# Optimization experiments

Measured on AMD Instinct MI355X. Metric: run time of the kernel, lower is better.

The kernel has to match this reference:

```python
import jax, jax.numpy as jnp
import numpy as np

EMB_DIM = 256
Q_DIM = 512
V_DIM = 512

def setup_inputs() -> dict:
    key = jax.random.key(0)
    ks = jax.random.split(key, 7)
    B, S = 8, 2048
    x = jax.random.normal(ks[0], (B, S, EMB_DIM), dtype=jnp.float32)
    s = 1.0 / np.sqrt(EMB_DIM)
    Wq = jax.random.normal(ks[1], (EMB_DIM, Q_DIM), dtype=jnp.float32) * s
    bq = jax.random.normal(ks[2], (Q_DIM,), dtype=jnp.float32) * 0.01
    Wk = jax.random.normal(ks[3], (EMB_DIM, Q_DIM), dtype=jnp.float32) * s
    bk = jax.random.normal(ks[4], (Q_DIM,), dtype=jnp.float32) * 0.01
    Wv = jax.random.normal(ks[5], (EMB_DIM, V_DIM), dtype=jnp.float32) * s
    bv = jax.random.normal(ks[6], (V_DIM,), dtype=jnp.float32) * 0.01
    return {"x": x, "Wq": Wq, "bq": bq, "Wk": Wk, "bk": bk, "Wv": Wv, "bv": bv}

def reference(x, Wq, bq, Wk, bk, Wv, bv):
    # q/k/v projections (torch Linear == x @ W + b with W stored [in, out] here)
    q = jax.nn.sigmoid(jnp.einsum('bse,eq->bsq', x, Wq) + bq)   # [B,S,Q]
    k = jnp.einsum('bse,eq->bsq', x, Wk) + bk                   # [B,S,Q]
    v = jnp.einsum('bse,ev->bsv', x, Wv) + bv                   # [B,S,V]
    scale = 1.0 / jnp.sqrt(jnp.float32(EMB_DIM))
    qk = jnp.einsum('bsq,btq->bst', q, k) * scale               # [B,S,S]
    qk = jax.nn.elu(qk)
    attn = jax.nn.softmax(qk, axis=-1)
    return jnp.einsum('bst,btv->bsv', attn, v)                  # [B,S,V]
```

## Files before the change

### kernel.cpp

```cpp
#include <hip/hip_runtime.h>
#include <hip/hip_bf16.h>
#include <math.h>

typedef unsigned short u16;
using short8 = __attribute__((ext_vector_type(8))) short;
using f32x4  = __attribute__((ext_vector_type(4))) float;

#define BK 32


__device__ __forceinline__ u16 f2bf(float f) {
  union { float f; unsigned u; } v; v.f = f;
  unsigned r = v.u + 0x7FFFu + ((v.u >> 16) & 1u);
  return (u16)(r >> 16);
}

__device__ __forceinline__ float fexp(float x) { return __expf(x); }

__device__ __forceinline__ void gld16(const void* g, void* l) {
  __builtin_amdgcn_global_load_lds(
      (const __attribute__((address_space(1))) void*)g,
      (__attribute__((address_space(3))) void*)l,
      16, 0, 0);
}


__device__ __forceinline__ void gemm_core4(const u16* __restrict__ Ag,
                                           const u16* __restrict__ Bg,
                                           int K, int lda, int ldb,
                                           u16* As, u16* Bs,
                                           f32x4 acc[4][4], int w, int l) {
  const int wm = (w & 1) << 6, wn = (w >> 1) << 6;
  const int ln = l & 15, lq = l >> 4;
  const int sr0 = w * 16 + (l >> 2);
  const int sr1 = 64 + sr0;
  const int skp = (l & 3) * 8;
  const int skg = ((l & 3) ^ ((l >> 3) & 3)) * 8;
  const int kro = (lq ^ ((ln >> 1) & 3)) * 8;

#pragma unroll
  for (int mt = 0; mt < 4; mt++)
#pragma unroll
    for (int nt = 0; nt < 4; nt++) acc[mt][nt] = (f32x4)0.0f;

  for (int k0 = 0; k0 < K; k0 += BK) {
    __syncthreads();
    gld16(Ag + (size_t)sr0 * lda + k0 + skg, As + sr0 * BK + skp);
    gld16(Ag + (size_t)sr1 * lda + k0 + skg, As + sr1 * BK + skp);
    gld16(Bg + (size_t)sr0 * ldb + k0 + skg, Bs + sr0 * BK + skp);
    gld16(Bg + (size_t)sr1 * ldb + k0 + skg, Bs + sr1 * BK + skp);
    __syncthreads();
    short8 af[4], bf[4];
#pragma unroll
    for (int mt = 0; mt < 4; mt++)
      af[mt] = *(const short8*)(As + (wm + mt * 16 + ln) * BK + kro);
#pragma unroll
    for (int nt = 0; nt < 4; nt++)
      bf[nt] = *(const short8*)(Bs + (wn + nt * 16 + ln) * BK + kro);
#pragma unroll
    for (int mt = 0; mt < 4; mt++)
#pragma unroll
      for (int nt = 0; nt < 4; nt++)
        acc[mt][nt] = __builtin_amdgcn_mfma_f32_16x16x32_bf16(
            af[mt], bf[nt], acc[mt][nt], 0, 0, 0);
  }
}


__global__ __launch_bounds__(256) void k_conv(
    const float* __restrict__ x, u16* __restrict__ xb,
    const float* __restrict__ Wq, const float* __restrict__ Wk,
    const float* __restrict__ Wv, const float* __restrict__ bq,
    const float* __restrict__ bk, const float* __restrict__ bv,
    u16* __restrict__ Wt, float* __restrict__ bcat,
    float* __restrict__ lsum) {
  const int bid = blockIdx.x;
  if (bid < 4096) {
    int i = bid * 256 + threadIdx.x;
    float4 v = ((const float4*)x)[i];
    ushort4 o;
    o.x = f2bf(v.x); o.y = f2bf(v.y); o.z = f2bf(v.z); o.w = f2bf(v.w);
    ((ushort4*)xb)[i] = o;
  } else if (bid < 5632) {
    int i = (bid - 4096) * 256 + threadIdx.x;
    int nn = i >> 8, e = i & 255;
    int sel = nn >> 9, c = nn & 511;
    const float* W = (sel == 0) ? Wq : (sel == 1) ? Wk : Wv;
    Wt[i] = f2bf(W[e * 512 + c]);
    if (e == 0) {
      const float* bb = (sel == 0) ? bq : (sel == 1) ? bk : bv;
      bcat[nn] = bb[c];
    }
  } else {
    int i = (bid - 5632) * 256 + threadIdx.x;
    lsum[i] = 0.0f;
  }
}


__global__ __launch_bounds__(256) void k_proj(
    const u16* __restrict__ xb, const u16* __restrict__ Wt,
    const float* __restrict__ bcat, u16* __restrict__ qb,
    u16* __restrict__ kb, u16* __restrict__ vtb) {
  __shared__ __align__(16) u16 As8[8 * 4096];
  __shared__ __align__(16) u16 Bs[4096];
  const int bm = blockIdx.y * 128;
  const int bnq = blockIdx.x;
  const int tid = threadIdx.x, w = tid >> 6, l = tid & 63;
  const int wm = (w & 1) << 6, wn = (w >> 1) << 6;
  const int ln = l & 15, lq = l >> 4;
  const int sr0 = w * 16 + (l >> 2);
  const int sr1 = 64 + sr0;
  const int skp = (l & 3) * 8;
  const int skg = ((l & 3) ^ ((l >> 3) & 3)) * 8;
  const int kro = (lq ^ ((ln >> 1) & 3)) * 8;

#pragma unroll
  for (int kw = 0; kw < 8; kw++) {
    gld16(xb + (size_t)(bm + sr0) * 256 + kw * 32 + skg,
          As8 + kw * 4096 + sr0 * BK + skp);
    gld16(xb + (size_t)(bm + sr1) * 256 + kw * 32 + skg,
          As8 + kw * 4096 + sr1 * BK + skp);
  }

  const int b = bm >> 11, t0 = bm & 2047;
  const int cb = bnq * 128;

  for (int p = 0; p < 3; p++) {
    const u16* Bg = Wt + (size_t)(p * 512 + cb) * 256;
    f32x4 acc[4][4];
#pragma unroll
    for (int mt = 0; mt < 4; mt++)
#pragma unroll
      for (int nt = 0; nt < 4; nt++) acc[mt][nt] = (f32x4)0.0f;

#pragma unroll
    for (int it = 0; it < 8; it++) {
      __syncthreads();
      gld16(Bg + (size_t)sr0 * 256 + it * 32 + skg, Bs + sr0 * BK + skp);
      gld16(Bg + (size_t)sr1 * 256 + it * 32 + skg, Bs + sr1 * BK + skp);
      __syncthreads();
      const u16* Aw = As8 + it * 4096;
      short8 af[4], bf[4];
#pragma unroll
      for (int mt = 0; mt < 4; mt++)
        af[mt] = *(const short8*)(Aw + (wm + mt * 16 + ln) * BK + kro);
#pragma unroll
      for (int nt = 0; nt < 4; nt++)
        bf[nt] = *(const short8*)(Bs + (wn + nt * 16 + ln) * BK + kro);
#pragma unroll
      for (int mt = 0; mt < 4; mt++)
#pragma unroll
        for (int nt = 0; nt < 4; nt++)
          acc[mt][nt] = __builtin_amdgcn_mfma_f32_16x16x32_bf16(
              af[mt], bf[nt], acc[mt][nt], 0, 0, 0);
    }

    if (p < 2) {
      u16* dst = p ? kb : qb;
#pragma unroll
      for (int mt = 0; mt < 4; mt++)
#pragma unroll
        for (int r = 0; r < 4; r++) {
          int row = bm + wm + mt * 16 + lq * 4 + r;
#pragma unroll
          for (int nt = 0; nt < 4; nt++) {
            int col = wn + nt * 16 + ln;
            float v = acc[mt][nt][r] + bcat[p * 512 + cb + col];
            float ov = (p == 0) ? __builtin_amdgcn_rcpf(1.0f + fexp(-v)) : v;
            dst[(size_t)row * 512 + cb + col] = f2bf(ov);
          }
        }
    } else {
      u16* tr = As8;
#pragma unroll
      for (int h = 0; h < 2; h++) {
        __syncthreads();
        if ((w & 1) == h) {
#pragma unroll
          for (int mt = 0; mt < 4; mt++)
#pragma unroll
            for (int nt = 0; nt < 4; nt++) {
              int c = wn + nt * 16 + ln;
              float bias = bcat[1024 + cb + c];
#pragma unroll
              for (int r = 0; r < 4; r++) {
                int lr = mt * 16 + lq * 4 + r;
                tr[c * 68 + lr] = f2bf(acc[mt][nt][r] + bias);
              }
            }
        }
        __syncthreads();
        int c2 = tid >> 1, half = tid & 1;
        size_t dbase = ((size_t)b * 512 + cb + c2) * 2048 + t0 + h * 64 + half * 32;
#pragma unroll
        for (int j = 0; j < 4; j++) {
          ushort4 a0 = *(const ushort4*)&tr[c2 * 68 + half * 32 + j * 8];
          ushort4 a1 = *(const ushort4*)&tr[c2 * 68 + half * 32 + j * 8 + 4];
          *(ushort4*)&vtb[dbase + j * 8] = a0;
          *(ushort4*)&vtb[dbase + j * 8 + 4] = a1;
        }
      }
    }
  }
}


__global__ __launch_bounds__(256, 4) void k_qk(const u16* __restrict__ qb,
                                               const u16* __restrict__ kb,
                                               u16* __restrict__ P,
                                               float* __restrict__ lsum) {
  __shared__ __align__(16) u16 As[128 * BK];
  __shared__ __align__(16) u16 Bs[128 * BK];
  const int bid = blockIdx.x;
  const int b = bid & 7, t = bid >> 3;
  const int bm = (t >> 4) * 128, bn = (t & 15) * 128;
  const size_t ob = (size_t)b * 2048 * 512;
  const int tid = threadIdx.x, w = tid >> 6, l = tid & 63;
  f32x4 acc[4][4];
  gemm_core4(qb + ob + (size_t)bm * 512, kb + ob + (size_t)bn * 512,
             512, 512, 512, As, Bs, acc, w, l);

  const int wm = (w & 1) << 6, wn = (w >> 1) << 6;
  const int ln = l & 15, lq = l >> 4;
  const float scale = 0.0625f;
#pragma unroll
  for (int mt = 0; mt < 4; mt++)
#pragma unroll
    for (int r = 0; r < 4; r++) {
      int row = bm + wm + mt * 16 + lq * 4 + r;
      float s = 0.0f;
#pragma unroll
      for (int nt = 0; nt < 4; nt++) {
        int col = bn + wn + nt * 16 + ln;
        float v = acc[mt][nt][r] * scale;
        float e = (v > 0.0f) ? v : (fexp(v) - 1.0f);
        float p = fexp(e);
        P[((size_t)b * 2048 + row) * 2048 + col] = f2bf(p);
        s += p;
      }
#pragma unroll
      for (int o = 1; o < 16; o <<= 1) s += __shfl_xor(s, o);
      if (ln == 0) atomicAdd(&lsum[b * 2048 + row], s);
    }
}


__global__ __launch_bounds__(256, 4) void k_pv(const u16* __restrict__ P,
                                               const u16* __restrict__ vtb,
                                               const float* __restrict__ lsum,
                                               float* __restrict__ out) {
  __shared__ __align__(16) u16 As[128 * BK];
  __shared__ __align__(16) u16 Bs[128 * BK];
  const int bid = blockIdx.x;
  const int b = bid & 7, t = bid >> 3;
  const int bm = (t >> 2) * 128, bn = (t & 3) * 128;
  const int tid = threadIdx.x, w = tid >> 6, l = tid & 63;
  f32x4 acc[4][4];
  gemm_core4(P  + (size_t)b * 2048 * 2048 + (size_t)bm * 2048,
             vtb + (size_t)b * 512 * 2048 + (size_t)bn * 2048,
             2048, 2048, 2048, As, Bs, acc, w, l);

  const int wm = (w & 1) << 6, wn = (w >> 1) << 6;
  const int ln = l & 15, lq = l >> 4;
#pragma unroll
  for (int mt = 0; mt < 4; mt++)
#pragma unroll
    for (int r = 0; r < 4; r++) {
      int row = bm + wm + mt * 16 + lq * 4 + r;
      float inv = 1.0f / lsum[b * 2048 + row];
#pragma unroll
      for (int nt = 0; nt < 4; nt++) {
        int col = bn + wn + nt * 16 + ln;
        out[((size_t)b * 2048 + row) * 512 + col] = acc[mt][nt][r] * inv;
      }
    }
}


extern "C" void kernel_launch(void* const* d_in, const int* in_sizes, int n_in,
                              void* d_out, int out_size, void* d_ws, size_t ws_size,
                              hipStream_t stream) {
  const float* x  = (const float*)d_in[0];
  const float* Wq = (const float*)d_in[1];
  const float* bq = (const float*)d_in[2];
  const float* Wk = (const float*)d_in[3];
  const float* bk = (const float*)d_in[4];
  const float* Wv = (const float*)d_in[5];
  const float* bv = (const float*)d_in[6];
  float* out = (float*)d_out;
  char* ws = (char*)d_ws;

  u16*  qb   = (u16*)(ws + 0);
  u16*  kb   = (u16*)(ws + 16777216);
  u16*  vtb  = (u16*)(ws + 33554432);
  float* lsum = (float*)(ws + 50331648);
  u16*  P    = (u16*)(ws + 50397184);
  u16*  xb   = (u16*)(ws + 50397184);
  u16*  Wt   = (u16*)(ws + 58785792);
  float* bcat = (float*)(ws + 59572224);

  k_conv<<<5696, 256, 0, stream>>>(x, xb, Wq, Wk, Wv, bq, bk, bv, Wt, bcat, lsum);
  k_proj<<<dim3(4, 128, 1), 256, 0, stream>>>(xb, Wt, bcat, qb, kb, vtb);
  k_qk<<<2048, 256, 0, stream>>>(qb, kb, P, lsum);
  k_pv<<<512, 256, 0, stream>>>(P, vtb, lsum, out);
}
```

Baseline: 213.3 us.

## Widen QK and PV tiles to 128x256 using 32x32x16 MFMA

Replaces the 128x128 GEMM core built on 16x16x32 MFMA with a 128x256 core built on 32x32x16 MFMA. Each wave now computes a 64x128 subtile, so fewer LDS reads are needed per MFMA and global data is reused more. The epilogues are remapped to the 32x32 accumulator layout, and grid sizes are halved. In exchange, register pressure rises (occupancy hint lowered to 2), and k_pv now launches only 256 blocks, which may underfill the GPU's CUs.

```diff
diff --git a/kernel.cpp b/kernel.cpp
--- a/kernel.cpp
+++ b/kernel.cpp
@@ -5,6 +5,7 @@
 typedef unsigned short u16;
 using short8 = __attribute__((ext_vector_type(8))) short;
 using f32x4  = __attribute__((ext_vector_type(4))) float;
+using f32x16 = __attribute__((ext_vector_type(16))) float;
 
 #define BK 32
 
@@ -25,44 +26,53 @@
 }
 
 
-__device__ __forceinline__ void gemm_core4(const u16* __restrict__ Ag,
-                                           const u16* __restrict__ Bg,
-                                           int K, int lda, int ldb,
-                                           u16* As, u16* Bs,
-                                           f32x4 acc[4][4], int w, int l) {
-  const int wm = (w & 1) << 6, wn = (w >> 1) << 6;
-  const int ln = l & 15, lq = l >> 4;
-  const int sr0 = w * 16 + (l >> 2);
-  const int sr1 = 64 + sr0;
+__device__ __forceinline__ void core_wide(const u16* __restrict__ Ag,
+                                          const u16* __restrict__ Bg,
+                                          int K, int lda, int ldb,
+                                          u16* As, u16* Bs,
+                                          f32x16 acc[2][4], int w, int l) {
+  const int ln = l & 31, l5 = l >> 5;
+  const int sr = w * 16 + (l >> 2);
   const int skp = (l & 3) * 8;
   const int skg = ((l & 3) ^ ((l >> 3) & 3)) * 8;
-  const int kro = (lq ^ ((ln >> 1) & 3)) * 8;
-
-#pragma unroll
-  for (int mt = 0; mt < 4; mt++)
-#pragma unroll
-    for (int nt = 0; nt < 4; nt++) acc[mt][nt] = (f32x4)0.0f;
+  const int wm = (w & 1) << 6, wn = (w >> 1) << 7;
+  const int g = (ln >> 1) & 3;
+  const int ko0 = (l5 ^ g) * 8;
+  const int ko1 = ((2 + l5) ^ g) * 8;
+
+#pragma unroll
+  for (int mt = 0; mt < 2; mt++)
+#pragma unroll
+    for (int nt = 0; nt < 4; nt++) acc[mt][nt] = (f32x16)0.0f;
 
   for (int k0 = 0; k0 < K; k0 += BK) {
     __syncthreads();
-    gld16(Ag + (size_t)sr0 * lda + k0 + skg, As + sr0 * BK + skp);
-    gld16(Ag + (size_t)sr1 * lda + k0 + skg, As + sr1 * BK + skp);
-    gld16(Bg + (size_t)sr0 * ldb + k0 + skg, Bs + sr0 * BK + skp);
-    gld16(Bg + (size_t)sr1 * ldb + k0 + skg, Bs + sr1 * BK + skp);
+    gld16(Ag + (size_t)sr * lda + k0 + skg, As + sr * BK + skp);
+    gld16(Ag + (size_t)(sr + 64) * lda + k0 + skg, As + (sr + 64) * BK + skp);
+#pragma unroll
+    for (int j = 0; j < 4; j++)
+      gld16(Bg + (size_t)(sr + 64 * j) * ldb + k0 + skg,
+            Bs + (sr + 64 * j) * BK + skp);
     __syncthreads();
-    short8 af[4], bf[4];
-#pragma unroll
-    for (int mt = 0; mt < 4; mt++)
-      af[mt] = *(const short8*)(As + (wm + mt * 16 + ln) * BK + kro);
-#pragma unroll
-    for (int nt = 0; nt < 4; nt++)
-      bf[nt] = *(const short8*)(Bs + (wn + nt * 16 + ln) * BK + kro);
-#pragma unroll
-    for (int mt = 0; mt < 4; mt++)
-#pragma unroll
-      for (int nt = 0; nt < 4; nt++)
-        acc[mt][nt] = __builtin_amdgcn_mfma_f32_16x16x32_bf16(
-            af[mt], bf[nt], acc[mt][nt], 0, 0, 0);
+    short8 af[2][2], bf[4][2];
+#pragma unroll
+    for (int mt = 0; mt < 2; mt++) {
+      af[mt][0] = *(const short8*)(As + (wm + mt * 32 + ln) * BK + ko0);
+      af[mt][1] = *(const short8*)(As + (wm + mt * 32 + ln) * BK + ko1);
+    }
+#pragma unroll
+    for (int nt = 0; nt < 4; nt++) {
+      bf[nt][0] = *(const short8*)(Bs + (wn + nt * 32 + ln) * BK + ko0);
+      bf[nt][1] = *(const short8*)(Bs + (wn + nt * 32 + ln) * BK + ko1);
+    }
+#pragma unroll
+    for (int kh = 0; kh < 2; kh++)
+#pragma unroll
+      for (int mt = 0; mt < 2; mt++)
+#pragma unroll
+        for (int nt = 0; nt < 4; nt++)
+          acc[mt][nt] = __builtin_amdgcn_mfma_f32_32x32x16_bf16(
+              af[mt][kh], bf[nt][kh], acc[mt][nt], 0, 0, 0);
   }
 }
 
@@ -206,33 +216,33 @@
 }
 
 
-__global__ __launch_bounds__(256, 4) void k_qk(const u16* __restrict__ qb,
+__global__ __launch_bounds__(256, 2) void k_qk(const u16* __restrict__ qb,
                                                const u16* __restrict__ kb,
                                                u16* __restrict__ P,
                                                float* __restrict__ lsum) {
   __shared__ __align__(16) u16 As[128 * BK];
-  __shared__ __align__(16) u16 Bs[128 * BK];
+  __shared__ __align__(16) u16 Bs[256 * BK];
   const int bid = blockIdx.x;
   const int b = bid & 7, t = bid >> 3;
-  const int bm = (t >> 4) * 128, bn = (t & 15) * 128;
+  const int bm = (t >> 3) * 128, bn = (t & 7) * 256;
   const size_t ob = (size_t)b * 2048 * 512;
   const int tid = threadIdx.x, w = tid >> 6, l = tid & 63;
-  f32x4 acc[4][4];
-  gemm_core4(qb + ob + (size_t)bm * 512, kb + ob + (size_t)bn * 512,
-             512, 512, 512, As, Bs, acc, w, l);
-
-  const int wm = (w & 1) << 6, wn = (w >> 1) << 6;
-  const int ln = l & 15, lq = l >> 4;
+  f32x16 acc[2][4];
+  core_wide(qb + ob + (size_t)bm * 512, kb + ob + (size_t)bn * 512,
+            512, 512, 512, As, Bs, acc, w, l);
+
+  const int wm = (w & 1) << 6, wn = (w >> 1) << 7;
+  const int ln = l & 31, l5 = l >> 5;
   const float scale = 0.0625f;
 #pragma unroll
-  for (int mt = 0; mt < 4; mt++)
-#pragma unroll
-    for (int r = 0; r < 4; r++) {
-      int row = bm + wm + mt * 16 + lq * 4 + r;
+  for (int mt = 0; mt < 2; mt++)
+#pragma unroll
+    for (int r = 0; r < 16; r++) {
+      int row = bm + wm + mt * 32 + (r & 3) + 8 * (r >> 2) + 4 * l5;
       float s = 0.0f;
 #pragma unroll
       for (int nt = 0; nt < 4; nt++) {
-        int col = bn + wn + nt * 16 + ln;
+        int col = bn + wn + nt * 32 + ln;
         float v = acc[mt][nt][r] * scale;
         float e = (v > 0.0f) ? v : (fexp(v) - 1.0f);
         float p = fexp(e);
@@ -240,38 +250,38 @@
         s += p;
       }
 #pragma unroll
-      for (int o = 1; o < 16; o <<= 1) s += __shfl_xor(s, o);
+      for (int o = 1; o < 32; o <<= 1) s += __shfl_xor(s, o);
       if (ln == 0) atomicAdd(&lsum[b * 2048 + row], s);
     }
 }
 
 
-__global__ __launch_bounds__(256, 4) void k_pv(const u16* __restrict__ P,
+__global__ __launch_bounds__(256, 2) void k_pv(const u16* __restrict__ P,
                                                const u16* __restrict__ vtb,
                                                const float* __restrict__ lsum,
                                                float* __restrict__ out) {
   __shared__ __align__(16) u16 As[128 * BK];
-  __shared__ __align__(16) u16 Bs[128 * BK];
+  __shared__ __align__(16) u16 Bs[256 * BK];
   const int bid = blockIdx.x;
   const int b = bid & 7, t = bid >> 3;
-  const int bm = (t >> 2) * 128, bn = (t & 3) * 128;
+  const int bm = (t >> 1) * 128, bn = (t & 1) * 256;
   const int tid = threadIdx.x, w = tid >> 6, l = tid & 63;
-  f32x4 acc[4][4];
-  gemm_core4(P  + (size_t)b * 2048 * 2048 + (size_t)bm * 2048,
-             vtb + (size_t)b * 512 * 2048 + (size_t)bn * 2048,
-             2048, 2048, 2048, As, Bs, acc, w, l);
-
-  const int wm = (w & 1) << 6, wn = (w >> 1) << 6;
-  const int ln = l & 15, lq = l >> 4;
-#pragma unroll
-  for (int mt = 0; mt < 4; mt++)
-#pragma unroll
-    for (int r = 0; r < 4; r++) {
-      int row = bm + wm + mt * 16 + lq * 4 + r;
+  f32x16 acc[2][4];
+  core_wide(P  + (size_t)b * 2048 * 2048 + (size_t)bm * 2048,
+            vtb + (size_t)b * 512 * 2048 + (size_t)bn * 2048,
+            2048, 2048, 2048, As, Bs, acc, w, l);
+
+  const int wm = (w & 1) << 6, wn = (w >> 1) << 7;
+  const int ln = l & 31, l5 = l >> 5;
+#pragma unroll
+  for (int mt = 0; mt < 2; mt++)
+#pragma unroll
+    for (int r = 0; r < 16; r++) {
+      int row = bm + wm + mt * 32 + (r & 3) + 8 * (r >> 2) + 4 * l5;
       float inv = 1.0f / lsum[b * 2048 + row];
 #pragma unroll
       for (int nt = 0; nt < 4; nt++) {
-        int col = bn + wn + nt * 16 + ln;
+        int col = bn + wn + nt * 32 + ln;
         out[((size_t)b * 2048 + row) * 512 + col] = acc[mt][nt][r] * inv;
       }
     }
@@ -302,6 +312,6 @@
 
   k_conv<<<5696, 256, 0, stream>>>(x, xb, Wq, Wk, Wv, bq, bk, bv, Wt, bcat, lsum);
   k_proj<<<dim3(4, 128, 1), 256, 0, stream>>>(xb, Wt, bcat, qb, kb, vtb);
-  k_qk<<<2048, 256, 0, stream>>>(qb, kb, P, lsum);
-  k_pv<<<512, 256, 0, stream>>>(P, vtb, lsum, out);
-}
+  k_qk<<<1024, 256, 0, stream>>>(qb, kb, P, lsum);
+  k_pv<<<256, 256, 0, stream>>>(P, vtb, lsum, out);
+}
```

Measured after the change: 229.5 us. 1.08x slower.
